# Optimization experiments

Hardware: AMD Instinct MI355X
Metric: run time of the kernel (lower is better)

The kernel has to match this reference:

```python
import jax, jax.numpy as jnp
import numpy as np

WIN = 1022       # window_length == frame_length == fft_length
HOP = 256        # hop_length
SIG_LEN = 33216  # signal_length
FACTOR = 2       # downsampling factor
T_IN = 127       # input STFT frames
B = 64
L_OLA = (T_IN - 1) * HOP + WIN  # 33278, length produced by inverse_stft

# indices kept after the strided deletion (evens < SIG_LEN, plus OLA tail beyond SIG_LEN)
KEEP = np.concatenate([np.arange(0, SIG_LEN, FACTOR), np.arange(SIG_LEN, L_OLA)])
L_OUT = KEEP.shape[0]                # 16670
T_OUT = 1 + (L_OUT - WIN) // HOP     # 62 output STFT frames

def _hann(n):
    # periodic Hann, matches tf.signal.hann_window default
    return (0.5 - 0.5 * np.cos(2.0 * np.pi * np.arange(n) / n)).astype(np.float32)

def _synth_window():
    # tf.signal.inverse_stft_window_fn(HOP): w / overlap-added w^2 (periodic form)
    w = _hann(WIN)
    d = w * w
    overlaps = -(-WIN // HOP)
    d = np.pad(d, (0, overlaps * HOP - WIN))
    d = d.reshape(-1, HOP).sum(0)      # per-phase sum of squares
    d = np.tile(d, overlaps)[:WIN]
    return (w / d).astype(np.float32)

WINDOW = jnp.asarray(_hann(WIN))
SYNTH = jnp.asarray(_synth_window())
OLA_IDX = jnp.asarray((np.arange(T_IN)[:, None] * HOP + np.arange(WIN)[None, :]).reshape(-1))
FRAME_IDX = jnp.asarray(np.arange(T_OUT)[:, None] * HOP + np.arange(WIN)[None, :])
KEEP_J = jnp.asarray(KEEP)

def setup_inputs() -> dict:
    key = jax.random.key(0)
    return {"inputs": jax.random.normal(key, (B, 512, T_IN, 2), dtype=jnp.float32)}

def reference(inputs):
    # inputs: [B, 512, T, 2] (real/imag stacked STFT)
    stfts = jax.lax.complex(inputs[..., 0], inputs[..., 1])   # [B, 512, T]
    stfts = jnp.transpose(stfts, (0, 2, 1))                   # [B, T, 512]
    # inverse_stft: irfft per frame, apply synthesis window, overlap-add
    frames = jnp.fft.irfft(stfts, n=WIN, axis=-1) * SYNTH
    b = frames.shape[0]
    sig = jnp.zeros((b, L_OLA), frames.dtype).at[:, OLA_IDX].add(frames.reshape(b, -1))
    # strided index deletion (the unstack/del/stack loop) == single gather
    sig = sig[:, KEEP_J]                                      # [B, 16670]
    # forward STFT
    fr = sig[:, FRAME_IDX] * WINDOW
    S = jnp.fft.rfft(fr, n=WIN, axis=-1)                      # [B, T_OUT, 512]
    S = jnp.transpose(S, (0, 2, 1))                           # [B, 512, T_OUT]
    return jnp.stack([jnp.real(S), jnp.imag(S)], axis=-1)     # [B, 512, T_OUT, 2]
```

## Files before the change

kernel.cpp:

```cpp
#include <hip/hip_runtime.h>


#define WIN       1022
#define HOP       256
#define T_IN      127
#define NB        64
#define NPAD      1024
#define NE        512
#define T_OUT     62
#define HALF_KEPT 16608
#define L_USE     16638
#define ROWS1     8128
#define ROWS1P    8192
#define ROWS2     3968
#define ROWS2P    4096
#define TWO_PI_F  6.28318530717958647692f

typedef _Float16 half8 __attribute__((ext_vector_type(8)));
typedef float    f32x4 __attribute__((ext_vector_type(4)));

__global__ __launch_bounds__(256) void prep(const float* __restrict__ in,
                                            _Float16* __restrict__ M1T,
                                            _Float16* __restrict__ M2T,
                                            _Float16* __restrict__ A1) {
    __shared__ float lds[32 * 254];
    int bx = blockIdx.x, tid = threadIdx.x;
    const float cc = TWO_PI_F / (float)WIN;

    if (bx < 4096) {
        int idx = bx * 256 + tid, j = idx >> 10, kk = idx & 1023;
        if ((j & 1) && j < 961) return;
        float v = 0.f;
        if (j < WIN) {
            float w = 0.5f - 0.5f * __cosf(cc * (float)j);
            float dd = 0.f;
            int p = j & (HOP - 1);
            for (int r = 0; r < 4; ++r) {
                int ix = p + HOP * r;
                if (ix < WIN) {
                    float wi = 0.5f - 0.5f * __cosf(cc * (float)ix);
                    dd += wi * wi;
                }
            }
            float synth = w / dd;
            int k = kk >> 1, c = kk & 1;
            if (!(c == 1 && (k == 0 || k == 511))) {
                float a = (k == 0 || k == 511) ? (1.f / (float)WIN) : (2.f / (float)WIN);
                int m = (k * j) % WIN;
                float s, co;
                __sincosf((float)m * cc, &s, &co);
                v = a * synth * (c == 0 ? co : -s);
            }
        }
        M1T[idx] = (_Float16)v;
        return;
    }
    if (bx < 8192) {
        int idx = (bx - 4096) * 256 + tid, col = idx >> 10, j = idx & 1023;
        float v = 0.f;
        if (j < WIN) {
            float w = 0.5f - 0.5f * __cosf(cc * (float)j);
            int k = col >> 1, c = col & 1;
            int m = (k * j) % WIN;
            float s, co;
            __sincosf((float)m * cc, &s, &co);
            v = w * (c == 0 ? co : -s);
        }
        M2T[idx] = (_Float16)v;
        return;
    }
    int bx2 = bx - 8192;
    int kt = bx2 >> 6, b = bx2 & 63;
    const float* base = in + ((size_t)b * 512 + kt * 32) * (T_IN * 2);
    for (int idx2 = tid; idx2 < 32 * 254; idx2 += 256)
        lds[idx2] = base[idx2];
    __syncthreads();
    for (int f = tid; f < T_IN * 64; f += 256) {
        int t = f >> 6, l = f & 63;
        int dk = l >> 1, c = l & 1;
        A1[(size_t)(b * T_IN + t) * NPAD + kt * 64 + l] =
            (_Float16)lds[dk * 254 + t * 2 + c];
    }
}


__device__ __forceinline__ void stage16(const void* g, void* l) {
    __builtin_amdgcn_global_load_lds(
        (const __attribute__((address_space(1))) unsigned int*)g,
        (__attribute__((address_space(3))) unsigned int*)l, 16, 0, 0);
}

template <bool G2>
__global__ __launch_bounds__(256) void gemm_mfma(const _Float16* __restrict__ A,
                                                 const _Float16* __restrict__ B0,
                                                 void* __restrict__ Cv) {
    constexpr int BPITCH = G2 ? NPAD : 2 * NPAD;
    constexpr int KTOT   = G2 ? NPAD : NE;
    __shared__ __align__(16) _Float16 As[128 * 64];
    __shared__ __align__(16) _Float16 Bs[64 * 64];

    int tid  = threadIdx.x;
    int lane = tid & 63, wave = tid >> 6;
    int quad = lane >> 4, l16 = lane & 15;
    int rowOff = (wave >> 1) * 64, colOff = (wave & 1) * 32;
    int rowBase = blockIdx.y * 128, colBase = blockIdx.x * 64;
    int kbase = G2 ? 0 : blockIdx.z * NE;

    const _Float16* Ag[4]; _Float16* Al[4];
    const _Float16* Bg[2]; _Float16* Bl[2];
#pragma unroll
    for (int u = 0; u < 4; ++u) {
        int f = u * 256 + tid, r = f >> 3, ko = (((f & 7) ^ (r & 7))) * 8;
        Ag[u] = A + (size_t)(rowBase + r) * NPAD + kbase + ko;
        Al[u] = As + f * 8;
    }
#pragma unroll
    for (int u = 0; u < 2; ++u) {
        int f = u * 256 + tid, r = f >> 3, ko = (((f & 7) ^ (r & 7))) * 8;
        Bg[u] = B0 + (size_t)(colBase + r) * BPITCH + kbase + ko;
        Bl[u] = Bs + f * 8;
    }

    f32x4 acc[4][2] = {};

    for (int k0 = 0; k0 < KTOT; k0 += 64) {
#pragma unroll
        for (int u = 0; u < 4; ++u) stage16(Ag[u] + k0, Al[u]);
#pragma unroll
        for (int u = 0; u < 2; ++u) stage16(Bg[u] + k0, Bl[u]);
        __syncthreads();

        half8 af[2][4], bf[2][2];
#pragma unroll
        for (int s = 0; s < 2; ++s) {
#pragma unroll
            for (int i = 0; i < 4; ++i) {
                int row = rowOff + i * 16 + l16;
                af[s][i] = *(const half8*)&As[row * 64 + (((s * 4 + quad) ^ (row & 7)) * 8)];
            }
#pragma unroll
            for (int j = 0; j < 2; ++j) {
                int row = colOff + j * 16 + l16;
                bf[s][j] = *(const half8*)&Bs[row * 64 + (((s * 4 + quad) ^ (row & 7)) * 8)];
            }
        }
#pragma unroll
        for (int s = 0; s < 2; ++s)
#pragma unroll
            for (int i = 0; i < 4; ++i)
#pragma unroll
                for (int j = 0; j < 2; ++j)
                    acc[i][j] = __builtin_amdgcn_mfma_f32_16x16x32_f16(af[s][i], bf[s][j], acc[i][j], 0, 0, 0);
        __syncthreads();
    }

#pragma unroll
    for (int i = 0; i < 4; ++i) {
#pragma unroll
        for (int j = 0; j < 2; ++j) {
            int col = colBase + colOff + j * 16 + l16;
            if (!G2) {
                _Float16* fe = (_Float16*)Cv + (size_t)blockIdx.z * ROWS1P * NE;
#pragma unroll
                for (int rr = 0; rr < 4; ++rr) {
                    int row = rowBase + rowOff + i * 16 + quad * 4 + rr;
                    fe[(size_t)row * NE + col] = (_Float16)acc[i][j][rr];
                }
            } else if (col < ROWS2) {
                int b = col / T_OUT, t2 = col % T_OUT;
#pragma unroll
                for (int rr = 0; rr < 4; rr += 2) {
                    int row = rowBase + rowOff + i * 16 + quad * 4 + rr;
                    int k = row >> 1;
                    float2 v = make_float2(acc[i][j][rr], acc[i][j][rr + 1]);
                    *(float2*)((float*)Cv + (((size_t)b * 512 + k) * T_OUT + t2) * 2) = v;
                }
            }
        }
    }
}

__global__ void ola_pack(const _Float16* __restrict__ fe0,
                         const _Float16* __restrict__ fe1,
                         const _Float16* __restrict__ A1,
                         const _Float16* __restrict__ M1T,
                         _Float16* __restrict__ fr) {
    int i = blockIdx.x * 256 + threadIdx.x;
    int b = blockIdx.y;
    if (i >= L_USE) return;

    float v = 0.f;
    if (i < HALF_KEPT) {
        int tmin = (i > 510) ? ((i - 383) >> 7) : 0;
        int tmax = i >> 7; if (tmax > T_IN - 1) tmax = T_IN - 1;
        for (int t = tmin; t <= tmax; ++t) {
            size_t idx = (size_t)(b * T_IN + t) * NE + (i - t * 128);
            v += (float)fe0[idx] + (float)fe1[idx];
        }
    } else {
        int s = i + HALF_KEPT;
        int p = s - 32256;
        if (!(s & 1)) {
            size_t idx = (size_t)(b * T_IN + 126) * NE + (p >> 1);
            v = (float)fe0[idx] + (float)fe1[idx];
        } else {
            const _Float16* ar = A1 + (size_t)(b * T_IN + 126) * NPAD;
            const _Float16* mr = M1T + (size_t)p * NPAD;
            float a0 = 0.f;
            for (int k = 0; k < NPAD; k += 8) {
                half8 av = *(const half8*)&ar[k];
                half8 mv = *(const half8*)&mr[k];
#pragma unroll
                for (int u = 0; u < 8; ++u)
                    a0 += (float)av[u] * (float)mv[u];
            }
            v = a0;
        }
    }

    _Float16 hv = (_Float16)v;
    int t2min = (i > WIN - 1) ? ((i - (WIN - 1) + HOP - 1) >> 8) : 0;
    int t2max = i >> 8; if (t2max > T_OUT - 1) t2max = T_OUT - 1;
    for (int t2 = t2min; t2 <= t2max; ++t2)
        fr[(size_t)(b * T_OUT + t2) * NPAD + (i - t2 * HOP)] = hv;
}


extern "C" void kernel_launch(void* const* d_in, const int* in_sizes, int n_in,
                              void* d_out, int out_size, void* d_ws, size_t ws_size,
                              hipStream_t stream) {
    const float* in = (const float*)d_in[0];
    float* out = (float*)d_out;
    char* ws = (char*)d_ws;

    _Float16* M1T = (_Float16*)ws;
    _Float16* M2T = M1T + (size_t)NPAD * NPAD;
    _Float16* A1  = M2T + (size_t)NPAD * NPAD;
    _Float16* fr  = A1 + (size_t)ROWS1P * NPAD;
    _Float16* fe  = fr + (size_t)ROWS2P * NPAD;

    prep<<<9216, 256, 0, stream>>>(in, M1T, M2T, A1);
    gemm_mfma<false><<<dim3(NE / 64, ROWS1P / 128, 2), 256, 0, stream>>>(A1, M1T, fe);
    ola_pack<<<dim3(65, NB), 256, 0, stream>>>(fe, fe + (size_t)ROWS1P * NE, A1, M1T, fr);
    gemm_mfma<true><<<dim3(ROWS2P / 64, NPAD / 128), 256, 0, stream>>>(M2T, fr, out);
}
```

Before: 146.5 us.

## Double-buffer LDS tiles in MFMA GEMM and trim padded column blocks

```diff
diff --git a/kernel.cpp b/kernel.cpp
--- a/kernel.cpp
+++ b/kernel.cpp
@@ -16,6 +16,10 @@
 #define ROWS2P    4096
 #define TWO_PI_F  6.28318530717958647692f
 
+#define WAIT_VM6   0x0F76
+#define WAIT_VM0   0x0F70
+#define WAIT_LGKM0 0xC07F
+
 typedef _Float16 half8 __attribute__((ext_vector_type(8)));
 typedef float    f32x4 __attribute__((ext_vector_type(4)));
 
@@ -96,8 +100,9 @@
                                                  void* __restrict__ Cv) {
     constexpr int BPITCH = G2 ? NPAD : 2 * NPAD;
     constexpr int KTOT   = G2 ? NPAD : NE;
-    __shared__ __align__(16) _Float16 As[128 * 64];
-    __shared__ __align__(16) _Float16 Bs[64 * 64];
+    constexpr int NITER  = KTOT / 64;
+    __shared__ __align__(16) _Float16 As[2][128 * 64];
+    __shared__ __align__(16) _Float16 Bs[2][64 * 64];
 
     int tid  = threadIdx.x;
     int lane = tid & 63, wave = tid >> 6;
@@ -106,29 +111,41 @@
     int rowBase = blockIdx.y * 128, colBase = blockIdx.x * 64;
     int kbase = G2 ? 0 : blockIdx.z * NE;
 
-    const _Float16* Ag[4]; _Float16* Al[4];
-    const _Float16* Bg[2]; _Float16* Bl[2];
+    const _Float16* Ag[4]; int Alo[4];
+    const _Float16* Bg[2]; int Blo[2];
 #pragma unroll
     for (int u = 0; u < 4; ++u) {
         int f = u * 256 + tid, r = f >> 3, ko = (((f & 7) ^ (r & 7))) * 8;
         Ag[u] = A + (size_t)(rowBase + r) * NPAD + kbase + ko;
-        Al[u] = As + f * 8;
+        Alo[u] = f * 8;
     }
 #pragma unroll
     for (int u = 0; u < 2; ++u) {
         int f = u * 256 + tid, r = f >> 3, ko = (((f & 7) ^ (r & 7))) * 8;
         Bg[u] = B0 + (size_t)(colBase + r) * BPITCH + kbase + ko;
-        Bl[u] = Bs + f * 8;
+        Blo[u] = f * 8;
     }
 
     f32x4 acc[4][2] = {};
 
-    for (int k0 = 0; k0 < KTOT; k0 += 64) {
-#pragma unroll
-        for (int u = 0; u < 4; ++u) stage16(Ag[u] + k0, Al[u]);
-#pragma unroll
-        for (int u = 0; u < 2; ++u) stage16(Bg[u] + k0, Bl[u]);
-        __syncthreads();
+#pragma unroll
+    for (int u = 0; u < 4; ++u) stage16(Ag[u], &As[0][Alo[u]]);
+#pragma unroll
+    for (int u = 0; u < 2; ++u) stage16(Bg[u], &Bs[0][Blo[u]]);
+
+    for (int it = 0; it < NITER; ++it) {
+        int cur = it & 1, nxt = cur ^ 1;
+        if (it + 1 < NITER) {
+            int k1 = (it + 1) * 64;
+#pragma unroll
+            for (int u = 0; u < 4; ++u) stage16(Ag[u] + k1, &As[nxt][Alo[u]]);
+#pragma unroll
+            for (int u = 0; u < 2; ++u) stage16(Bg[u] + k1, &Bs[nxt][Blo[u]]);
+            __builtin_amdgcn_s_waitcnt(WAIT_VM6);
+        } else {
+            __builtin_amdgcn_s_waitcnt(WAIT_VM0);
+        }
+        __builtin_amdgcn_s_barrier();
 
         half8 af[2][4], bf[2][2];
 #pragma unroll
@@ -136,12 +153,12 @@
 #pragma unroll
             for (int i = 0; i < 4; ++i) {
                 int row = rowOff + i * 16 + l16;
-                af[s][i] = *(const half8*)&As[row * 64 + (((s * 4 + quad) ^ (row & 7)) * 8)];
+                af[s][i] = *(const half8*)&As[cur][row * 64 + (((s * 4 + quad) ^ (row & 7)) * 8)];
             }
 #pragma unroll
             for (int j = 0; j < 2; ++j) {
                 int row = colOff + j * 16 + l16;
-                bf[s][j] = *(const half8*)&Bs[row * 64 + (((s * 4 + quad) ^ (row & 7)) * 8)];
+                bf[s][j] = *(const half8*)&Bs[cur][row * 64 + (((s * 4 + quad) ^ (row & 7)) * 8)];
             }
         }
 #pragma unroll
@@ -151,7 +168,9 @@
 #pragma unroll
                 for (int j = 0; j < 2; ++j)
                     acc[i][j] = __builtin_amdgcn_mfma_f32_16x16x32_f16(af[s][i], bf[s][j], acc[i][j], 0, 0, 0);
-        __syncthreads();
+
+        __builtin_amdgcn_s_waitcnt(WAIT_LGKM0);
+        __builtin_amdgcn_s_barrier();
     }
 
 #pragma unroll
@@ -166,7 +185,7 @@
                     int row = rowBase + rowOff + i * 16 + quad * 4 + rr;
                     fe[(size_t)row * NE + col] = (_Float16)acc[i][j][rr];
                 }
-            } else if (col < ROWS2) {
+            } else {
                 int b = col / T_OUT, t2 = col % T_OUT;
 #pragma unroll
                 for (int rr = 0; rr < 4; rr += 2) {
@@ -242,5 +261,5 @@
     prep<<<9216, 256, 0, stream>>>(in, M1T, M2T, A1);
     gemm_mfma<false><<<dim3(NE / 64, ROWS1P / 128, 2), 256, 0, stream>>>(A1, M1T, fe);
     ola_pack<<<dim3(65, NB), 256, 0, stream>>>(fe, fe + (size_t)ROWS1P * NE, A1, M1T, fr);
-    gemm_mfma<true><<<dim3(ROWS2P / 64, NPAD / 128), 256, 0, stream>>>(M2T, fr, out);
-}
+    gemm_mfma<true><<<dim3(ROWS2 / 64, NPAD / 128), 256, 0, stream>>>(M2T, fr, out);
+}
```

Result: no change. 148.5 us (+1.3%).
